# Optimization experiments

Hardware: AMD Instinct MI355X
Metric: run time of the kernel (lower is better)

The kernel has to match this reference:

```python
import jax, jax.numpy as jnp
import numpy as np

B = 16384
D = 128
N_LAYER = 2
USER_NUM, ITEM_NUM, ENTITY_NUM = 100000, 50000, 50000
H1, H2 = 256, 128  # hidden_layers


def setup_inputs() -> dict:
    key = jax.random.key(0)
    ks = jax.random.split(key, 20)
    inp = {
        'user_ids': jax.random.randint(ks[0], (B,), 0, USER_NUM),
        'item_ids': jax.random.randint(ks[1], (B,), 0, ITEM_NUM),
        'rec_target': jax.random.uniform(ks[2], (B,), dtype=jnp.float32),
        # embedding tables
        'user_tbl': jax.random.normal(ks[3], (USER_NUM, D), dtype=jnp.float32) * 0.02,
        'item_tbl': jax.random.normal(ks[4], (ITEM_NUM, D), dtype=jnp.float32) * 0.02,
        'entity_tbl': jax.random.normal(ks[5], (ENTITY_NUM, D), dtype=jnp.float32) * 0.02,
        # cross-compress weights (torch.rand -> uniform)
        'w_vv': jax.random.uniform(ks[6], (D, 1), dtype=jnp.float32),
        'w_ev': jax.random.uniform(ks[7], (D, 1), dtype=jnp.float32),
        'w_ve': jax.random.uniform(ks[8], (D, 1), dtype=jnp.float32),
        'w_ee': jax.random.uniform(ks[9], (D, 1), dtype=jnp.float32),
        'bias_v': jax.random.uniform(ks[10], (1,), dtype=jnp.float32),
        'bias_e': jax.random.uniform(ks[11], (1,), dtype=jnp.float32),
        # user low MLP (Linear D->D)
        'Wu': jax.random.normal(ks[12], (D, D), dtype=jnp.float32) * 0.05,
        'bu': jnp.zeros((D,), dtype=jnp.float32),
        # rec MLP: 2D -> H1 -> H2 -> 1
        'W1': jax.random.normal(ks[13], (2 * D, H1), dtype=jnp.float32) * 0.05,
        'b1': jnp.zeros((H1,), dtype=jnp.float32),
        'W2': jax.random.normal(ks[14], (H1, H2), dtype=jnp.float32) * 0.05,
        'b2': jnp.zeros((H2,), dtype=jnp.float32),
        'W3': jax.random.normal(ks[15], (H2, 1), dtype=jnp.float32) * 0.05,
        'b3': jnp.zeros((1,), dtype=jnp.float32),
    }
    return inp


def _cross_compress(item, head, w_vv, w_ev, w_ve, w_ee, bias_v, bias_e):
    # c[b,i,j] = item[b,i]*head[b,j]; c_t[b,i,j] = head[b,i]*item[b,j]
    # (c @ w)[b,i] = item[b,i] * (head @ w)[b]; (c_t @ w)[b,i] = head[b,i] * (item @ w)[b]
    hv = head @ w_vv  # [B,1]
    iv = item @ w_ev  # [B,1]
    he = head @ w_ve  # [B,1]
    ie = item @ w_ee  # [B,1]
    item_c = item * hv + head * iv + bias_v
    head_c = item * he + head * ie + bias_e
    return item_c, head_c


def reference(user_ids, item_ids, rec_target, user_tbl, item_tbl, entity_tbl,
              w_vv, w_ev, w_ve, w_ee, bias_v, bias_e,
              Wu, bu, W1, b1, W2, b2, W3, b3):
    # train_type == 'rec' branch
    user_embed = user_tbl[user_ids]      # [B, D]
    item_embed = item_tbl[item_ids]      # [B, D]
    head_embed = entity_tbl[item_ids]    # [B, D]
    for _ in range(N_LAYER):
        user_embed = jax.nn.relu(user_embed @ Wu + bu)  # linear_layer (dropout=identity at eval)
        item_embed, head_embed = _cross_compress(
            item_embed, head_embed, w_vv, w_ev, w_ve, w_ee, bias_v, bias_e)
    high = jnp.concatenate([user_embed, item_embed], axis=1)  # [B, 2D]
    h = jax.nn.relu(high @ W1 + b1)
    h = jax.nn.relu(h @ W2 + b2)
    rec_out = jax.nn.relu(h @ W3 + b3)  # [B, 1]
    return rec_out[:, 0], rec_target
```

## Files before the change

### kernel.cpp

```cpp
#include <hip/hip_runtime.h>

#define BATCH 16384
#define DIM 128

typedef __attribute__((ext_vector_type(8))) short short8;
typedef __attribute__((ext_vector_type(4))) float floatx4;

__device__ __forceinline__ ushort f2bf(float f) {
    union { float f; uint u; } c; c.f = f;
    return (ushort)((c.u + 0x7FFFu + ((c.u >> 16) & 1u)) >> 16);
}
__device__ __forceinline__ float bf2f(ushort h) {
    union { uint u; float f; } c; c.u = ((uint)h) << 16;
    return c.f;
}
__device__ __forceinline__ ushort4 f4_to_bf4(float4 v) {
    return make_ushort4(f2bf(v.x), f2bf(v.y), f2bf(v.z), f2bf(v.w));
}

__device__ __forceinline__ int slot_idx(int KT, int m, int k) {
    return (((m >> 4) * KT + (k >> 5)) << 6) + (((k >> 3) & 3) << 4) + (m & 15);
}

__global__ __launch_bounds__(256) void convert_kernel(
    const float* __restrict__ Wu, const float* __restrict__ W1,
    const float* __restrict__ W2, short8* __restrict__ WF)
{
    const int f    = blockIdx.x * 4 + (threadIdx.x >> 6);
    const int lane = threadIdx.x & 63;
    const int q = lane >> 4, r = lane & 15;
    const float* W; int N, nt, kf, fl; short8* dst;
    if (f < 32)       { W = Wu; N = 128; fl = f;       nt = fl >> 2; kf = fl & 3; dst = WF;         }
    else if (f < 160) { W = W1; N = 256; fl = f - 32;  nt = fl >> 3; kf = fl & 7; dst = WF + 2048;  }
    else              { W = W2; N = 128; fl = f - 160; nt = fl >> 3; kf = fl & 7; dst = WF + 10240; }
    const int n = nt * 16 + r, k0 = kf * 32 + q * 8;
    short8 v;
    #pragma unroll
    for (int j = 0; j < 8; ++j)
        v[j] = (short)f2bf(W[(size_t)(k0 + j) * N + n]);
    dst[fl * 64 + lane] = v;
}

template<int KF, int NT, int DKT>
__device__ __forceinline__ void layer_mfma(
    const short8* __restrict__ src, const short8* __restrict__ WF,
    const float* __restrict__ bias, ushort* __restrict__ dst, int tid)
{
    const int wave = tid >> 6, lane = tid & 63;
    const int q = lane >> 4, r = lane & 15;
    short8 a[2][KF];
    #pragma unroll
    for (int mt = 0; mt < 2; ++mt)
        #pragma unroll
        for (int kf = 0; kf < KF; ++kf)
            a[mt][kf] = src[(mt * KF + kf) * 64 + lane];
    #pragma unroll
    for (int nt = wave; nt < NT; nt += 4) {
        const int col = nt * 16 + r;
        short8 b[KF];
        #pragma unroll
        for (int kf = 0; kf < KF; ++kf)
            b[kf] = WF[(nt * KF + kf) * 64 + lane];
        const float bs = bias[col];
        const int kc = col >> 5, qc = (col >> 3) & 3, e = col & 7;
        #pragma unroll
        for (int mt = 0; mt < 2; ++mt) {
            floatx4 acc = {0.f, 0.f, 0.f, 0.f};
            #pragma unroll
            for (int kf = 0; kf < KF; ++kf)
                acc = __builtin_amdgcn_mfma_f32_16x16x32_bf16(a[mt][kf], b[kf], acc, 0, 0, 0);
            #pragma unroll
            for (int rr = 0; rr < 4; ++rr) {
                const int rlow = q * 4 + rr;
                dst[(size_t)((((mt * DKT + kc) << 6) + (qc << 4) + rlow) * 8 + e)] =
                    f2bf(fmaxf(acc[rr] + bs, 0.f));
            }
        }
    }
}

__global__ __launch_bounds__(256) void fused_kernel(
    const int* __restrict__ user_ids, const int* __restrict__ item_ids,
    const float* __restrict__ rec_target,
    const float* __restrict__ user_tbl, const float* __restrict__ item_tbl,
    const float* __restrict__ entity_tbl,
    const float* __restrict__ w_vv, const float* __restrict__ w_ev,
    const float* __restrict__ w_ve, const float* __restrict__ w_ee,
    const float* __restrict__ bias_v, const float* __restrict__ bias_e,
    const short8* __restrict__ WF, const float* __restrict__ bu,
    const float* __restrict__ b1, const float* __restrict__ b2,
    const float* __restrict__ W3, const float* __restrict__ b3,
    float* __restrict__ out)
{
    __shared__ short8 sU0[512];
    __shared__ short8 sU1[512];
    __shared__ short8 sHI[1024];
    __shared__ short8 sH1[1024];
    __shared__ short8 sH2[512];

    const int r0  = blockIdx.x * 32;
    const int tid = threadIdx.x;
    const int row = tid >> 3, l = tid & 7;

    if (tid < 32) out[BATCH + r0 + tid] = rec_target[r0 + tid];

    {
        const int uid = user_ids[r0 + row];
        const float4* src = (const float4*)(user_tbl + (size_t)uid * DIM + l * 16);
        ushort* p = (ushort*)sU0;
        #pragma unroll
        for (int i = 0; i < 4; ++i) {
            const int col = l * 16 + i * 4;
            *(ushort4*)&p[slot_idx(4, row, col) * 8 + (col & 7)] = f4_to_bf4(src[i]);
        }
    }

    {
        const int id = item_ids[r0 + row];
        const float4* ip = (const float4*)(item_tbl   + (size_t)id * DIM + l * 16);
        const float4* hp = (const float4*)(entity_tbl + (size_t)id * DIM + l * 16);
        float4 it4[4], hd4[4];
        #pragma unroll
        for (int i = 0; i < 4; ++i) { it4[i] = ip[i]; hd4[i] = hp[i]; }
        const float bv = bias_v[0], be = bias_e[0];
        #pragma unroll
        for (int lay = 0; lay < 2; ++lay) {
            float hv = 0.f, iv = 0.f, he = 0.f, ie = 0.f;
            #pragma unroll
            for (int i = 0; i < 4; ++i) {
                float4 wvv = ((const float4*)w_vv)[l * 4 + i];
                float4 wev = ((const float4*)w_ev)[l * 4 + i];
                float4 wve = ((const float4*)w_ve)[l * 4 + i];
                float4 wee = ((const float4*)w_ee)[l * 4 + i];
                hv += hd4[i].x * wvv.x + hd4[i].y * wvv.y + hd4[i].z * wvv.z + hd4[i].w * wvv.w;
                iv += it4[i].x * wev.x + it4[i].y * wev.y + it4[i].z * wev.z + it4[i].w * wev.w;
                he += hd4[i].x * wve.x + hd4[i].y * wve.y + hd4[i].z * wve.z + hd4[i].w * wve.w;
                ie += it4[i].x * wee.x + it4[i].y * wee.y + it4[i].z * wee.z + it4[i].w * wee.w;
            }
            hv += __shfl_xor(hv, 1); hv += __shfl_xor(hv, 2); hv += __shfl_xor(hv, 4);
            iv += __shfl_xor(iv, 1); iv += __shfl_xor(iv, 2); iv += __shfl_xor(iv, 4);
            he += __shfl_xor(he, 1); he += __shfl_xor(he, 2); he += __shfl_xor(he, 4);
            ie += __shfl_xor(ie, 1); ie += __shfl_xor(ie, 2); ie += __shfl_xor(ie, 4);
            #pragma unroll
            for (int i = 0; i < 4; ++i) {
                float4 t = it4[i], h = hd4[i];
                it4[i].x = t.x * hv + h.x * iv + bv;  hd4[i].x = t.x * he + h.x * ie + be;
                it4[i].y = t.y * hv + h.y * iv + bv;  hd4[i].y = t.y * he + h.y * ie + be;
                it4[i].z = t.z * hv + h.z * iv + bv;  hd4[i].z = t.z * he + h.z * ie + be;
                it4[i].w = t.w * hv + h.w * iv + bv;  hd4[i].w = t.w * he + h.w * ie + be;
            }
        }
        ushort* p = (ushort*)sHI;
        #pragma unroll
        for (int i = 0; i < 4; ++i) {
            const int col = 128 + l * 16 + i * 4;
            *(ushort4*)&p[slot_idx(8, row, col) * 8 + (col & 7)] = f4_to_bf4(it4[i]);
        }
    }
    __syncthreads();

    layer_mfma<4, 8, 4>(sU0, WF,          bu, (ushort*)sU1, tid);
    __syncthreads();
    layer_mfma<4, 8, 8>(sU1, WF,          bu, (ushort*)sHI, tid);
    __syncthreads();
    layer_mfma<8, 16, 8>(sHI, WF + 2048,  b1, (ushort*)sH1, tid);
    __syncthreads();
    layer_mfma<8, 8, 4>(sH1, WF + 10240,  b2, (ushort*)sH2, tid);
    __syncthreads();

    {
        float p = 0.f;
        #pragma unroll
        for (int i = 0; i < 2; ++i) {
            const int c8 = l * 2 + i;
            short8 h = sH2[(((row >> 4) * 4 + (c8 >> 2)) << 6) + ((c8 & 3) << 4) + (row & 15)];
            float4 w0 = ((const float4*)W3)[c8 * 2];
            float4 w1 = ((const float4*)W3)[c8 * 2 + 1];
            p += bf2f((ushort)h[0]) * w0.x + bf2f((ushort)h[1]) * w0.y
               + bf2f((ushort)h[2]) * w0.z + bf2f((ushort)h[3]) * w0.w
               + bf2f((ushort)h[4]) * w1.x + bf2f((ushort)h[5]) * w1.y
               + bf2f((ushort)h[6]) * w1.z + bf2f((ushort)h[7]) * w1.w;
        }
        p += __shfl_xor(p, 1); p += __shfl_xor(p, 2); p += __shfl_xor(p, 4);
        if (l == 0) out[r0 + row] = fmaxf(p + b3[0], 0.f);
    }
}

extern "C" void kernel_launch(void* const* d_in, const int* in_sizes, int n_in,
                              void* d_out, int out_size, void* d_ws, size_t ws_size,
                              hipStream_t stream)
{
    const int*   user_ids   = (const int*)  d_in[0];
    const int*   item_ids   = (const int*)  d_in[1];
    const float* rec_target = (const float*)d_in[2];
    const float* user_tbl   = (const float*)d_in[3];
    const float* item_tbl   = (const float*)d_in[4];
    const float* entity_tbl = (const float*)d_in[5];
    const float* w_vv       = (const float*)d_in[6];
    const float* w_ev       = (const float*)d_in[7];
    const float* w_ve       = (const float*)d_in[8];
    const float* w_ee       = (const float*)d_in[9];
    const float* bias_v     = (const float*)d_in[10];
    const float* bias_e     = (const float*)d_in[11];
    const float* Wu         = (const float*)d_in[12];
    const float* bu         = (const float*)d_in[13];
    const float* W1         = (const float*)d_in[14];
    const float* b1         = (const float*)d_in[15];
    const float* W2         = (const float*)d_in[16];
    const float* b2         = (const float*)d_in[17];
    const float* W3         = (const float*)d_in[18];
    const float* b3         = (const float*)d_in[19];
    float* out = (float*)d_out;

    short8* WF = (short8*)d_ws;

    convert_kernel<<<56, 256, 0, stream>>>(Wu, W1, W2, WF);
    fused_kernel<<<BATCH / 32, 256, 0, stream>>>(
        user_ids, item_ids, rec_target, user_tbl, item_tbl, entity_tbl,
        w_vv, w_ev, w_ve, w_ee, bias_v, bias_e,
        WF, bu, b1, b2, W3, b3, out);
}
```

Baseline: 155.9 us.

## Process 64 rows per block and ping-pong two shared buffers

Each block now handles 64 batch rows instead of 32, with four threads per row. Each MFMA wave therefore reuses every weight fragment it loads across four M-tiles instead of two, halving weight traffic per row. The five separate LDS buffers become two 32 KB ping-pong buffers with a uniform 8-k-tile stride, and launch bounds request two blocks per CU. The cost is fewer blocks (256, about one wave of CUs), more registers per thread, and less latency hiding for the embedding gathers.

Result: slower. 164.5 us (+5.5%).

```diff
diff --git a/kernel.cpp b/kernel.cpp
--- a/kernel.cpp
+++ b/kernel.cpp
@@ -18,8 +18,8 @@
     return make_ushort4(f2bf(v.x), f2bf(v.y), f2bf(v.z), f2bf(v.w));
 }
 
-__device__ __forceinline__ int slot_idx(int KT, int m, int k) {
-    return (((m >> 4) * KT + (k >> 5)) << 6) + (((k >> 3) & 3) << 4) + (m & 15);
+__device__ __forceinline__ int slot_idx(int m, int k) {
+    return (((m >> 4) * 8 + (k >> 5)) << 6) + (((k >> 3) & 3) << 4) + (m & 15);
 }
 
 __global__ __launch_bounds__(256) void convert_kernel(
@@ -41,19 +41,19 @@
     dst[fl * 64 + lane] = v;
 }
 
-template<int KF, int NT, int DKT>
+template<int KF, int NT>
 __device__ __forceinline__ void layer_mfma(
     const short8* __restrict__ src, const short8* __restrict__ WF,
     const float* __restrict__ bias, ushort* __restrict__ dst, int tid)
 {
     const int wave = tid >> 6, lane = tid & 63;
     const int q = lane >> 4, r = lane & 15;
-    short8 a[2][KF];
+    short8 a[4][KF];
     #pragma unroll
-    for (int mt = 0; mt < 2; ++mt)
+    for (int mt = 0; mt < 4; ++mt)
         #pragma unroll
         for (int kf = 0; kf < KF; ++kf)
-            a[mt][kf] = src[(mt * KF + kf) * 64 + lane];
+            a[mt][kf] = src[(mt * 8 + kf) * 64 + lane];
     #pragma unroll
     for (int nt = wave; nt < NT; nt += 4) {
         const int col = nt * 16 + r;
@@ -64,7 +64,7 @@
         const float bs = bias[col];
         const int kc = col >> 5, qc = (col >> 3) & 3, e = col & 7;
         #pragma unroll
-        for (int mt = 0; mt < 2; ++mt) {
+        for (int mt = 0; mt < 4; ++mt) {
             floatx4 acc = {0.f, 0.f, 0.f, 0.f};
             #pragma unroll
             for (int kf = 0; kf < KF; ++kf)
@@ -72,14 +72,14 @@
             #pragma unroll
             for (int rr = 0; rr < 4; ++rr) {
                 const int rlow = q * 4 + rr;
-                dst[(size_t)((((mt * DKT + kc) << 6) + (qc << 4) + rlow) * 8 + e)] =
+                dst[(size_t)((((mt * 8 + kc) << 6) + (qc << 4) + rlow) * 8 + e)] =
                     f2bf(fmaxf(acc[rr] + bs, 0.f));
             }
         }
     }
 }
 
-__global__ __launch_bounds__(256) void fused_kernel(
+__global__ __launch_bounds__(256, 2) void fused_kernel(
     const int* __restrict__ user_ids, const int* __restrict__ item_ids,
     const float* __restrict__ rec_target,
     const float* __restrict__ user_tbl, const float* __restrict__ item_tbl,
@@ -92,57 +92,54 @@
     const float* __restrict__ W3, const float* __restrict__ b3,
     float* __restrict__ out)
 {
-    __shared__ short8 sU0[512];
-    __shared__ short8 sU1[512];
-    __shared__ short8 sHI[1024];
-    __shared__ short8 sH1[1024];
-    __shared__ short8 sH2[512];
-
-    const int r0  = blockIdx.x * 32;
+    __shared__ short8 sA[2048];
+    __shared__ short8 sB[2048];
+
+    const int r0  = blockIdx.x * 64;
     const int tid = threadIdx.x;
-    const int row = tid >> 3, l = tid & 7;
-
-    if (tid < 32) out[BATCH + r0 + tid] = rec_target[r0 + tid];
+    const int row = tid >> 2, l = tid & 3;
+
+    if (tid < 64) out[BATCH + r0 + tid] = rec_target[r0 + tid];
 
     {
         const int uid = user_ids[r0 + row];
-        const float4* src = (const float4*)(user_tbl + (size_t)uid * DIM + l * 16);
-        ushort* p = (ushort*)sU0;
-        #pragma unroll
-        for (int i = 0; i < 4; ++i) {
-            const int col = l * 16 + i * 4;
-            *(ushort4*)&p[slot_idx(4, row, col) * 8 + (col & 7)] = f4_to_bf4(src[i]);
+        const float4* src = (const float4*)(user_tbl + (size_t)uid * DIM + l * 32);
+        ushort* p = (ushort*)sA;
+        #pragma unroll
+        for (int i = 0; i < 8; ++i) {
+            const int col = l * 32 + i * 4;
+            *(ushort4*)&p[slot_idx(row, col) * 8 + (col & 7)] = f4_to_bf4(src[i]);
         }
     }
 
     {
         const int id = item_ids[r0 + row];
-        const float4* ip = (const float4*)(item_tbl   + (size_t)id * DIM + l * 16);
-        const float4* hp = (const float4*)(entity_tbl + (size_t)id * DIM + l * 16);
-        float4 it4[4], hd4[4];
-        #pragma unroll
-        for (int i = 0; i < 4; ++i) { it4[i] = ip[i]; hd4[i] = hp[i]; }
+        const float4* ip = (const float4*)(item_tbl   + (size_t)id * DIM + l * 32);
+        const float4* hp = (const float4*)(entity_tbl + (size_t)id * DIM + l * 32);
+        float4 it4[8], hd4[8];
+        #pragma unroll
+        for (int i = 0; i < 8; ++i) { it4[i] = ip[i]; hd4[i] = hp[i]; }
         const float bv = bias_v[0], be = bias_e[0];
         #pragma unroll
         for (int lay = 0; lay < 2; ++lay) {
             float hv = 0.f, iv = 0.f, he = 0.f, ie = 0.f;
             #pragma unroll
-            for (int i = 0; i < 4; ++i) {
-                float4 wvv = ((const float4*)w_vv)[l * 4 + i];
-                float4 wev = ((const float4*)w_ev)[l * 4 + i];
-                float4 wve = ((const float4*)w_ve)[l * 4 + i];
-                float4 wee = ((const float4*)w_ee)[l * 4 + i];
+            for (int i = 0; i < 8; ++i) {
+                float4 wvv = ((const float4*)w_vv)[l * 8 + i];
+                float4 wev = ((const float4*)w_ev)[l * 8 + i];
+                float4 wve = ((const float4*)w_ve)[l * 8 + i];
+                float4 wee = ((const float4*)w_ee)[l * 8 + i];
                 hv += hd4[i].x * wvv.x + hd4[i].y * wvv.y + hd4[i].z * wvv.z + hd4[i].w * wvv.w;
                 iv += it4[i].x * wev.x + it4[i].y * wev.y + it4[i].z * wev.z + it4[i].w * wev.w;
                 he += hd4[i].x * wve.x + hd4[i].y * wve.y + hd4[i].z * wve.z + hd4[i].w * wve.w;
                 ie += it4[i].x * wee.x + it4[i].y * wee.y + it4[i].z * wee.z + it4[i].w * wee.w;
             }
-            hv += __shfl_xor(hv, 1); hv += __shfl_xor(hv, 2); hv += __shfl_xor(hv, 4);
-            iv += __shfl_xor(iv, 1); iv += __shfl_xor(iv, 2); iv += __shfl_xor(iv, 4);
-            he += __shfl_xor(he, 1); he += __shfl_xor(he, 2); he += __shfl_xor(he, 4);
-            ie += __shfl_xor(ie, 1); ie += __shfl_xor(ie, 2); ie += __shfl_xor(ie, 4);
-            #pragma unroll
-            for (int i = 0; i < 4; ++i) {
+            hv += __shfl_xor(hv, 1); hv += __shfl_xor(hv, 2);
+            iv += __shfl_xor(iv, 1); iv += __shfl_xor(iv, 2);
+            he += __shfl_xor(he, 1); he += __shfl_xor(he, 2);
+            ie += __shfl_xor(ie, 1); ie += __shfl_xor(ie, 2);
+            #pragma unroll
+            for (int i = 0; i < 8; ++i) {
                 float4 t = it4[i], h = hd4[i];
                 it4[i].x = t.x * hv + h.x * iv + bv;  hd4[i].x = t.x * he + h.x * ie + be;
                 it4[i].y = t.y * hv + h.y * iv + bv;  hd4[i].y = t.y * he + h.y * ie + be;
@@ -150,30 +147,30 @@
                 it4[i].w = t.w * hv + h.w * iv + bv;  hd4[i].w = t.w * he + h.w * ie + be;
             }
         }
-        ushort* p = (ushort*)sHI;
-        #pragma unroll
-        for (int i = 0; i < 4; ++i) {
-            const int col = 128 + l * 16 + i * 4;
-            *(ushort4*)&p[slot_idx(8, row, col) * 8 + (col & 7)] = f4_to_bf4(it4[i]);
-        }
-    }
-    __syncthreads();
-
-    layer_mfma<4, 8, 4>(sU0, WF,          bu, (ushort*)sU1, tid);
-    __syncthreads();
-    layer_mfma<4, 8, 8>(sU1, WF,          bu, (ushort*)sHI, tid);
-    __syncthreads();
-    layer_mfma<8, 16, 8>(sHI, WF + 2048,  b1, (ushort*)sH1, tid);
-    __syncthreads();
-    layer_mfma<8, 8, 4>(sH1, WF + 10240,  b2, (ushort*)sH2, tid);
+        ushort* p = (ushort*)sA;
+        #pragma unroll
+        for (int i = 0; i < 8; ++i) {
+            const int col = 128 + l * 32 + i * 4;
+            *(ushort4*)&p[slot_idx(row, col) * 8 + (col & 7)] = f4_to_bf4(it4[i]);
+        }
+    }
+    __syncthreads();
+
+    layer_mfma<4, 8>(sA, WF,          bu, (ushort*)sB, tid);
+    __syncthreads();
+    layer_mfma<4, 8>(sB, WF,          bu, (ushort*)sA, tid);
+    __syncthreads();
+    layer_mfma<8, 16>(sA, WF + 2048,  b1, (ushort*)sB, tid);
+    __syncthreads();
+    layer_mfma<8, 8>(sB, WF + 10240,  b2, (ushort*)sA, tid);
     __syncthreads();
 
     {
         float p = 0.f;
         #pragma unroll
-        for (int i = 0; i < 2; ++i) {
-            const int c8 = l * 2 + i;
-            short8 h = sH2[(((row >> 4) * 4 + (c8 >> 2)) << 6) + ((c8 & 3) << 4) + (row & 15)];
+        for (int i = 0; i < 4; ++i) {
+            const int c8 = l * 4 + i;
+            short8 h = sA[(((row >> 4) * 8 + (c8 >> 2)) << 6) + ((c8 & 3) << 4) + (row & 15)];
             float4 w0 = ((const float4*)W3)[c8 * 2];
             float4 w1 = ((const float4*)W3)[c8 * 2 + 1];
             p += bf2f((ushort)h[0]) * w0.x + bf2f((ushort)h[1]) * w0.y
@@ -181,7 +178,7 @@
                + bf2f((ushort)h[4]) * w1.x + bf2f((ushort)h[5]) * w1.y
                + bf2f((ushort)h[6]) * w1.z + bf2f((ushort)h[7]) * w1.w;
         }
-        p += __shfl_xor(p, 1); p += __shfl_xor(p, 2); p += __shfl_xor(p, 4);
+        p += __shfl_xor(p, 1); p += __shfl_xor(p, 2);
         if (l == 0) out[r0 + row] = fmaxf(p + b3[0], 0.f);
     }
 }
@@ -215,7 +212,7 @@
     short8* WF = (short8*)d_ws;
 
     convert_kernel<<<56, 256, 0, stream>>>(Wu, W1, W2, WF);
-    fused_kernel<<<BATCH / 32, 256, 0, stream>>>(
+    fused_kernel<<<BATCH / 64, 256, 0, stream>>>(
         user_ids, item_ids, rec_target, user_tbl, item_tbl, entity_tbl,
         w_vv, w_ev, w_ve, w_ee, bias_v, bias_e,
         WF, bu, b1, b2, W3, b3, out);
```
